# Kernel tuning notes

Measured on AMD Instinct MI355X. Metric: run time of the kernel, lower is better.

The kernel has to match this reference:

```python
import jax, jax.numpy as jnp
import numpy as np

B, N, HID = 2, 512, 768
BIAF = 256
CLS = 14
CH = 32
SIZE_DIM = 25
N_POS = 30
HSZ = 2 * (BIAF + 1) + SIZE_DIM


def setup_inputs() -> dict:
    key = jax.random.key(0)
    ks = jax.random.split(key, 16)
    s = 0.02
    return {
        "x": jax.random.normal(ks[0], (B, N, HID), jnp.float32),
        "y": jax.random.normal(ks[1], (B, N, HID), jnp.float32),
        "z": jax.random.normal(ks[2], (B, N, N, CH), jnp.float32),
        "mlp1_w": jax.random.normal(ks[3], (BIAF, HID), jnp.float32) * s,
        "mlp1_b": jnp.zeros((BIAF,), jnp.float32),
        "mlp2_w": jax.random.normal(ks[4], (BIAF, HID), jnp.float32) * s,
        "mlp2_b": jnp.zeros((BIAF,), jnp.float32),
        "head_w": jax.random.normal(ks[5], (BIAF, HID), jnp.float32) * s,
        "head_b": jnp.zeros((BIAF,), jnp.float32),
        "tail_w": jax.random.normal(ks[6], (BIAF, HID), jnp.float32) * s,
        "tail_b": jnp.zeros((BIAF,), jnp.float32),
        "biaf_W": jax.random.normal(ks[7], (CLS, BIAF + 1, BIAF + 1), jnp.float32) * s,
        "W": jax.random.normal(ks[8], (CLS, HSZ), jnp.float32) * s,
        "size_emb": jax.random.normal(ks[9], (N_POS, SIZE_DIM), jnp.float32) * s,
    }


def reference(x, y, z, mlp1_w, mlp1_b, mlp2_w, mlp2_b, head_w, head_b,
              tail_w, tail_b, biaf_W, W, size_emb):
    # MLP branches (dropout=0 at eval; torch GELU is exact erf)
    h = jax.nn.gelu(x @ mlp1_w.T + mlp1_b, approximate=False)   # (b,m,BIAF)
    t = jax.nn.gelu(y @ mlp2_w.T + mlp2_b, approximate=False)   # (b,n,BIAF)
    ones = jnp.ones(h.shape[:-1] + (1,), h.dtype)
    h1 = jnp.concatenate([h, ones], -1)                          # (b,m,BIAF+1)
    t1 = jnp.concatenate([t, ones], -1)                          # (b,n,BIAF+1)
    # Biaffine with bias_x=bias_y=True -> (b,cls,m,n)
    o1 = jnp.einsum('bmi,kij,bnj->bkmn', h1, biaf_W, t1)

    # head/tail MLPs with LeakyReLU(0.01), then append 1-column
    head = jax.nn.leaky_relu(x @ head_w.T + head_b, 0.01)
    tail = jax.nn.leaky_relu(x @ tail_w.T + tail_b, 0.01)
    head = jnp.concatenate([head, ones], -1)                     # (b,m,BIAF+1)
    tail = jnp.concatenate([tail, ones], -1)                     # (b,n,BIAF+1)

    # einsum('bmnh,kh->bkmn', cat([head_m, tail_n, size_mn]), W) decomposed so
    # the (b,m,n,HSZ) pairwise tensor is never materialized (same math).
    d = head.shape[-1]
    Wh, Wt, Ws = W[:, :d], W[:, d:2 * d], W[:, 2 * d:]
    n = x.shape[1]
    ar = jnp.arange(n)
    ids = jnp.clip(ar[None, :] - ar[:, None], -N_POS // 2, N_POS // 2 - 1) + N_POS // 2
    se = size_emb[ids]                                           # (m,n,SIZE_DIM)
    o3 = (jnp.einsum('bmh,kh->bkm', head, Wh)[:, :, :, None]
          + jnp.einsum('bnh,kh->bkn', tail, Wt)[:, :, None, :]
          + jnp.einsum('mnh,kh->kmn', se, Ws)[None])
    return o1 + o3
```

## Files before the change

### kernel.cpp

```cpp
#include <hip/hip_runtime.h>
#include <hip/hip_bf16.h>
#include <math.h>

#define BDIM 2
#define NDIM 512
#define HID 768
#define BIAF 256
#define CLS 14
#define DD 257
#define NPOS 30
#define SDIM 25
#define HSZ 539
#define PK 288
#define PJ 384

typedef unsigned short ushort_t;
typedef __attribute__((ext_vector_type(8))) short short8;
typedef __attribute__((ext_vector_type(4))) float floatx4;

#define MFMA16(a, b, c) __builtin_amdgcn_mfma_f32_16x16x32_bf16((a), (b), (c), 0, 0, 0)

__device__ inline float bf2f(ushort_t u) {
    union { unsigned int i; float f; } c; c.i = ((unsigned)u) << 16; return c.f;
}
__device__ inline ushort_t f2bf(float f) {
    __hip_bfloat16 h = __float2bfloat16(f);
    return *(ushort_t*)&h;
}

__device__ inline void split8(const float* v, short8& hi, short8& lo) {
    #pragma unroll
    for (int j = 0; j < 8; ++j) {
        ushort_t h = f2bf(v[j]);
        float hf = bf2f(h);
        ((short*)&hi)[j] = (short)h;
        ((short*)&lo)[j] = (short)f2bf(v[j] - hf);
    }
}

__global__ __launch_bounds__(256) void repack_t(
    const float* __restrict__ biafW, ushort_t* __restrict__ packW)
{
    __shared__ float tile[32][33];
    const int i0 = blockIdx.x * 32;
    const int j0 = blockIdx.y * 32;
    const int k  = blockIdx.z;
    const int r8 = threadIdx.x >> 5;
    const int c  = threadIdx.x & 31;
    #pragma unroll
    for (int rr = 0; rr < 4; ++rr) {
        int r = rr * 8 + r8;
        int gi = i0 + r, gj = j0 + c;
        tile[r][c] = (gi < DD && gj < DD) ? biafW[((size_t)k * DD + gi) * DD + gj] : 0.f;
    }
    __syncthreads();
    #pragma unroll
    for (int rr = 0; rr < 4; ++rr) {
        int jr = rr * 8 + r8;
        packW[((size_t)k * PJ + (j0 + jr)) * PK + i0 + c] = f2bf(tile[c][jr]);
    }
}

__global__ void fill_pads(ushort_t* __restrict__ h1hi, ushort_t* __restrict__ h1lo,
                          ushort_t* __restrict__ t1hi, ushort_t* __restrict__ t1lo) {
    int idx = blockIdx.x * 256 + threadIdx.x;
    int plane = idx >> 15;
    int tok = (idx >> 5) & 1023;
    int c   = 256 + (idx & 31);
    ushort_t* dst = (plane == 0) ? h1hi : (plane == 1) ? h1lo : (plane == 2) ? t1hi : t1lo;
    ushort_t val = (c == 256 && (plane == 0 || plane == 2)) ? (ushort_t)0x3F80 : (ushort_t)0;
    dst[(size_t)tok * PK + c] = val;
}

__global__ __launch_bounds__(256) void proj_mfma(
    const float* __restrict__ x, const float* __restrict__ y,
    const float* __restrict__ m1w, const float* __restrict__ m1b,
    const float* __restrict__ m2w, const float* __restrict__ m2b,
    const float* __restrict__ hw,  const float* __restrict__ hb,
    const float* __restrict__ tw,  const float* __restrict__ tb,
    ushort_t* __restrict__ h1hi, ushort_t* __restrict__ h1lo,
    ushort_t* __restrict__ t1hi, ushort_t* __restrict__ t1lo,
    float* __restrict__ headf, float* __restrict__ tailf)
{
    const int bx = blockIdx.x;
    const int proj = bx >> 6;
    const int mt = (bx >> 2) & 15;
    const int ft = bx & 3;
    const int wave = threadIdx.x >> 6, L = threadIdx.x & 63;
    const int quad = L >> 4, l16 = L & 15;
    const int m0w = mt * 64 + wave * 16;
    const int f0 = ft * 64;

    const float* src  = (proj == 1) ? y : x;
    const float* wmat = (proj == 0) ? m1w : (proj == 1) ? m2w : (proj == 2) ? hw : tw;
    const float* bias = (proj == 0) ? m1b : (proj == 1) ? m2b : (proj == 2) ? hb : tb;

    const float* arow = src + (size_t)(m0w + l16) * HID + quad * 8;

    floatx4 acc[4];
    #pragma unroll
    for (int nf = 0; nf < 4; ++nf)
        #pragma unroll
        for (int r = 0; r < 4; ++r) acc[nf][r] = 0.f;

    for (int k0 = 0; k0 < HID; k0 += 32) {
        float av[8];
        *(float4*)&av[0] = *(const float4*)(arow + k0);
        *(float4*)&av[4] = *(const float4*)(arow + k0 + 4);
        short8 ahi, alo;
        split8(av, ahi, alo);
        #pragma unroll
        for (int nf = 0; nf < 4; ++nf) {
            const float* brow = wmat + (size_t)(f0 + nf * 16 + l16) * HID + quad * 8 + k0;
            float bv[8];
            *(float4*)&bv[0] = *(const float4*)(brow);
            *(float4*)&bv[4] = *(const float4*)(brow + 4);
            short8 bhi, blo;
            split8(bv, bhi, blo);
            acc[nf] = MFMA16(ahi, bhi, acc[nf]);
            acc[nf] = MFMA16(alo, bhi, acc[nf]);
            acc[nf] = MFMA16(ahi, blo, acc[nf]);
        }
    }

    #pragma unroll
    for (int nf = 0; nf < 4; ++nf) {
        int feat = f0 + nf * 16 + l16;
        float bv = bias[feat];
        #pragma unroll
        for (int r = 0; r < 4; ++r) {
            int tok = m0w + quad * 4 + r;
            float v = acc[nf][r] + bv;
            if (proj == 0) {
                float g = 0.5f * v * (1.0f + erff(v * 0.70710678118654752f));
                ushort_t h = f2bf(g);
                h1hi[(size_t)tok * PK + feat] = h;
                h1lo[(size_t)tok * PK + feat] = f2bf(g - bf2f(h));
            } else if (proj == 1) {
                float g = 0.5f * v * (1.0f + erff(v * 0.70710678118654752f));
                ushort_t h = f2bf(g);
                t1hi[(size_t)tok * PK + feat] = h;
                t1lo[(size_t)tok * PK + feat] = f2bf(g - bf2f(h));
            } else if (proj == 2) {
                headf[(size_t)tok * 256 + feat] = (v >= 0.f) ? v : 0.01f * v;
            } else {
                tailf[(size_t)tok * 256 + feat] = (v >= 0.f) ? v : 0.01f * v;
            }
        }
    }
}

__global__ __launch_bounds__(256) void hk_tk_kernel(
    const float* __restrict__ headf, const float* __restrict__ tailf,
    const float* __restrict__ W,
    float* __restrict__ hk, float* __restrict__ tk)
{
    int p = blockIdx.x * 256 + threadIdx.x;
    int which = p >> 14;
    int idx = p & 16383;
    int tok = idx >> 4;
    int k = idx & 15;
    if (k >= CLS) return;
    const float* row = (which ? tailf : headf) + (size_t)tok * 256;
    const float* wr = W + (size_t)k * HSZ + (which ? DD : 0);
    float acc = 0.f;
    for (int f4 = 0; f4 < 64; ++f4) {
        float4 rv = *(const float4*)(row + f4 * 4);
        acc += rv.x * wr[f4*4] + rv.y * wr[f4*4+1] + rv.z * wr[f4*4+2] + rv.w * wr[f4*4+3];
    }
    acc += wr[256];
    float* dst = which ? tk : hk;
    dst[(size_t)(tok >> 9) * CLS * NDIM + (size_t)k * NDIM + (tok & 511)] = acc;
}

__global__ void sk_kernel(const float* __restrict__ semb, const float* __restrict__ W,
                          float* __restrict__ sk)
{
    int idx = blockIdx.x * 256 + threadIdx.x;
    if (idx < CLS * NPOS) {
        int k = idx / NPOS, d = idx % NPOS;
        float acc = 0.f;
        for (int h = 0; h < SDIM; ++h)
            acc += semb[d*SDIM + h] * W[k*HSZ + 2*DD + h];
        sk[idx] = acc;
    }
}

__global__ __launch_bounds__(256) void mb_mfma(
    const ushort_t* __restrict__ h1hi, const ushort_t* __restrict__ h1lo,
    const ushort_t* __restrict__ packW,
    ushort_t* __restrict__ Ab)
{
    const int jt = blockIdx.x, mt = blockIdx.y, bk = blockIdx.z;
    const int b = bk / CLS, k = bk % CLS;
    const int wave = threadIdx.x >> 6, L = threadIdx.x & 63;
    const int quad = L >> 4, l16 = L & 15;
    const int m0 = mt * 128 + (wave >> 1) * 64;
    const int j0 = jt * 128 + (wave & 1) * 64;
    const size_t abase = (size_t)b * NDIM * PK;
    const ushort_t* BT = packW + (size_t)k * PJ * PK;

    size_t aoff[4]; size_t boff[4];
    #pragma unroll
    for (int i = 0; i < 4; ++i) aoff[i] = abase + (size_t)(m0 + i * 16 + l16) * PK + quad * 8;
    #pragma unroll
    for (int i = 0; i < 4; ++i) boff[i] = (size_t)(j0 + i * 16 + l16) * PK + quad * 8;

    floatx4 acc[4][4];
    #pragma unroll
    for (int mi = 0; mi < 4; ++mi)
        #pragma unroll
        for (int ni = 0; ni < 4; ++ni)
            #pragma unroll
            for (int r = 0; r < 4; ++r) acc[mi][ni][r] = 0.f;

    for (int k0 = 0; k0 < PK; k0 += 32) {
        short8 ahi[4], alo[4], bb[4];
        #pragma unroll
        for (int i = 0; i < 4; ++i) {
            ahi[i] = *(const short8*)(h1hi + aoff[i] + k0);
            alo[i] = *(const short8*)(h1lo + aoff[i] + k0);
            bb[i]  = *(const short8*)(BT + boff[i] + k0);
        }
        #pragma unroll
        for (int mi = 0; mi < 4; ++mi)
            #pragma unroll
            for (int ni = 0; ni < 4; ++ni) {
                acc[mi][ni] = MFMA16(ahi[mi], bb[ni], acc[mi][ni]);
                acc[mi][ni] = MFMA16(alo[mi], bb[ni], acc[mi][ni]);
            }
    }

    ushort_t* Aout = Ab + (size_t)bk * NDIM * PK;
    #pragma unroll
    for (int mi = 0; mi < 4; ++mi) {
        #pragma unroll
        for (int r = 0; r < 4; ++r) {
            int row = m0 + mi * 16 + quad * 4 + r;
            #pragma unroll
            for (int ni = 0; ni < 4; ++ni) {
                int col = j0 + ni * 16 + l16;
                if (col < PK) Aout[(size_t)row * PK + col] = f2bf(acc[mi][ni][r]);
            }
        }
    }
}

__global__ __launch_bounds__(256) void mo_mfma(
    const ushort_t* __restrict__ Ab,
    const ushort_t* __restrict__ t1hi, const ushort_t* __restrict__ t1lo,
    const float* __restrict__ hk, const float* __restrict__ tk,
    const float* __restrict__ sk,
    float* __restrict__ out)
{
    __shared__ float skr[NPOS];
    const int nt = blockIdx.x, mt = blockIdx.y, bk = blockIdx.z;
    const int b = bk / CLS, k = bk % CLS;
    if (threadIdx.x < NPOS) skr[threadIdx.x] = sk[k * NPOS + threadIdx.x];
    __syncthreads();
    const int wave = threadIdx.x >> 6, L = threadIdx.x & 63;
    const int quad = L >> 4, l16 = L & 15;
    const int m0 = mt * 128 + (wave >> 1) * 64;
    const int n0 = nt * 128 + (wave & 1) * 64;
    const ushort_t* A = Ab + (size_t)bk * NDIM * PK;
    const size_t tbase = (size_t)b * NDIM * PK;

    size_t aoff[4]; size_t boff[4];
    #pragma unroll
    for (int i = 0; i < 4; ++i) aoff[i] = (size_t)(m0 + i * 16 + l16) * PK + quad * 8;
    #pragma unroll
    for (int i = 0; i < 4; ++i) boff[i] = tbase + (size_t)(n0 + i * 16 + l16) * PK + quad * 8;

    floatx4 acc[4][4];
    #pragma unroll
    for (int mi = 0; mi < 4; ++mi)
        #pragma unroll
        for (int ni = 0; ni < 4; ++ni)
            #pragma unroll
            for (int r = 0; r < 4; ++r) acc[mi][ni][r] = 0.f;

    for (int k0 = 0; k0 < PK; k0 += 32) {
        short8 a[4], bhi[4], blo[4];
        #pragma unroll
        for (int i = 0; i < 4; ++i) {
            a[i]   = *(const short8*)(A + aoff[i] + k0);
            bhi[i] = *(const short8*)(t1hi + boff[i] + k0);
            blo[i] = *(const short8*)(t1lo + boff[i] + k0);
        }
        #pragma unroll
        for (int mi = 0; mi < 4; ++mi)
            #pragma unroll
            for (int ni = 0; ni < 4; ++ni) {
                acc[mi][ni] = MFMA16(a[mi], bhi[ni], acc[mi][ni]);
                acc[mi][ni] = MFMA16(a[mi], blo[ni], acc[mi][ni]);
            }
    }

    const size_t obase = (size_t)bk * NDIM;
    #pragma unroll
    for (int mi = 0; mi < 4; ++mi) {
        #pragma unroll
        for (int r = 0; r < 4; ++r) {
            int row = m0 + mi * 16 + quad * 4 + r;
            float hv = hk[obase + row];
            #pragma unroll
            for (int ni = 0; ni < 4; ++ni) {
                int col = n0 + ni * 16 + l16;
                int d = col - row; d = d < -15 ? -15 : (d > 14 ? 14 : d); d += 15;
                out[(obase + row) * NDIM + col] = acc[mi][ni][r] + hv + tk[obase + col] + skr[d];
            }
        }
    }
}

extern "C" void kernel_launch(void* const* d_in, const int* in_sizes, int n_in,
                              void* d_out, int out_size, void* d_ws, size_t ws_size,
                              hipStream_t stream) {
    const float* x    = (const float*)d_in[0];
    const float* y    = (const float*)d_in[1];
    const float* m1w  = (const float*)d_in[3];
    const float* m1b  = (const float*)d_in[4];
    const float* m2w  = (const float*)d_in[5];
    const float* m2b  = (const float*)d_in[6];
    const float* hw   = (const float*)d_in[7];
    const float* hb   = (const float*)d_in[8];
    const float* tw   = (const float*)d_in[9];
    const float* tb   = (const float*)d_in[10];
    const float* biafW= (const float*)d_in[11];
    const float* W    = (const float*)d_in[12];
    const float* semb = (const float*)d_in[13];

    char* p = (char*)d_ws;
    float* hk   = (float*)p;                    p += 57344;
    float* tk   = (float*)p;                    p += 57344;
    float* skp  = (float*)p;                    p += 2048;
    float* headf= (float*)p;                    p += 1048576;
    float* tailf= (float*)p;                    p += 1048576;
    ushort_t* h1hi = (ushort_t*)p;              p += 589824;
    ushort_t* h1lo = (ushort_t*)p;              p += 589824;
    ushort_t* t1hi = (ushort_t*)p;              p += 589824;
    ushort_t* t1lo = (ushort_t*)p;              p += 589824;
    ushort_t* packW= (ushort_t*)p;              p += 3096576;
    ushort_t* Abuf = (ushort_t*)p;              p += 8257536;

    repack_t<<<dim3(9, 12, CLS), 256, 0, stream>>>(biafW, packW);
    fill_pads<<<512, 256, 0, stream>>>(h1hi, h1lo, t1hi, t1lo);
    proj_mfma<<<256, 256, 0, stream>>>(x, y, m1w, m1b, m2w, m2b,
                                       hw, hb, tw, tb,
                                       h1hi, h1lo, t1hi, t1lo, headf, tailf);
    hk_tk_kernel<<<128, 256, 0, stream>>>(headf, tailf, W, hk, tk);
    sk_kernel<<<2, 256, 0, stream>>>(semb, W, skp);
    mb_mfma<<<dim3(3, 4, BDIM*CLS), 256, 0, stream>>>(h1hi, h1lo, packW, Abuf);
    mo_mfma<<<dim3(4, 4, BDIM*CLS), 256, 0, stream>>>(Abuf, t1hi, t1lo, hk, tk, skp,
                                                      (float*)d_out);
}
```

Baseline: 217.1 us.

## Fuse biaffine stages via LDS intermediate and pre-split projection weights to bf16

Merges the two biaffine GEMM kernels into one kernel. Each block computes a 64-row slice of h1·W_k into shared memory, then multiplies it by t1 directly, so the global bf16 intermediate buffer and one launch are gone. It also adds a kernel that pre-splits the four projection weight matrices into bf16 hi/lo planes, so proj_mfma loads them instead of converting per block. In exchange, the first stage is now recomputed for every 64-row slice at full width, giving a smaller grid (224 blocks) with more registers per wave. The per-wave column assignment is also uneven (5 vs 4 fragments).

Result: slower. 259.5 us (+19.5%).

```diff
diff --git a/kernel.cpp b/kernel.cpp
--- a/kernel.cpp
+++ b/kernel.cpp
@@ -61,6 +61,21 @@
     }
 }
 
+__global__ __launch_bounds__(256) void wsplit(
+    const float* __restrict__ m1w, const float* __restrict__ m2w,
+    const float* __restrict__ hw,  const float* __restrict__ tw,
+    ushort_t* __restrict__ whi, ushort_t* __restrict__ wlo)
+{
+    int idx = blockIdx.x * 256 + threadIdx.x;
+    int mat = idx / (BIAF * HID);
+    int rem = idx % (BIAF * HID);
+    const float* src = (mat == 0) ? m1w : (mat == 1) ? m2w : (mat == 2) ? hw : tw;
+    float v = src[rem];
+    ushort_t h = f2bf(v);
+    whi[idx] = h;
+    wlo[idx] = f2bf(v - bf2f(h));
+}
+
 __global__ void fill_pads(ushort_t* __restrict__ h1hi, ushort_t* __restrict__ h1lo,
                           ushort_t* __restrict__ t1hi, ushort_t* __restrict__ t1lo) {
     int idx = blockIdx.x * 256 + threadIdx.x;
@@ -74,10 +89,9 @@
 
 __global__ __launch_bounds__(256) void proj_mfma(
     const float* __restrict__ x, const float* __restrict__ y,
-    const float* __restrict__ m1w, const float* __restrict__ m1b,
-    const float* __restrict__ m2w, const float* __restrict__ m2b,
-    const float* __restrict__ hw,  const float* __restrict__ hb,
-    const float* __restrict__ tw,  const float* __restrict__ tb,
+    const ushort_t* __restrict__ whi, const ushort_t* __restrict__ wlo,
+    const float* __restrict__ m1b, const float* __restrict__ m2b,
+    const float* __restrict__ hb,  const float* __restrict__ tb,
     ushort_t* __restrict__ h1hi, ushort_t* __restrict__ h1lo,
     ushort_t* __restrict__ t1hi, ushort_t* __restrict__ t1lo,
     float* __restrict__ headf, float* __restrict__ tailf)
@@ -92,10 +106,10 @@
     const int f0 = ft * 64;
 
     const float* src  = (proj == 1) ? y : x;
-    const float* wmat = (proj == 0) ? m1w : (proj == 1) ? m2w : (proj == 2) ? hw : tw;
     const float* bias = (proj == 0) ? m1b : (proj == 1) ? m2b : (proj == 2) ? hb : tb;
 
     const float* arow = src + (size_t)(m0w + l16) * HID + quad * 8;
+    const size_t wbase = (size_t)proj * BIAF * HID;
 
     floatx4 acc[4];
     #pragma unroll
@@ -111,12 +125,9 @@
         split8(av, ahi, alo);
         #pragma unroll
         for (int nf = 0; nf < 4; ++nf) {
-            const float* brow = wmat + (size_t)(f0 + nf * 16 + l16) * HID + quad * 8 + k0;
-            float bv[8];
-            *(float4*)&bv[0] = *(const float4*)(brow);
-            *(float4*)&bv[4] = *(const float4*)(brow + 4);
-            short8 bhi, blo;
-            split8(bv, bhi, blo);
+            size_t boff = wbase + (size_t)(f0 + nf * 16 + l16) * HID + quad * 8 + k0;
+            short8 bhi = *(const short8*)(whi + boff);
+            short8 blo = *(const short8*)(wlo + boff);
             acc[nf] = MFMA16(ahi, bhi, acc[nf]);
             acc[nf] = MFMA16(alo, bhi, acc[nf]);
             acc[nf] = MFMA16(ahi, blo, acc[nf]);
@@ -186,114 +197,109 @@
     }
 }
 
-__global__ __launch_bounds__(256) void mb_mfma(
+__global__ __launch_bounds__(256) void fused_out(
     const ushort_t* __restrict__ h1hi, const ushort_t* __restrict__ h1lo,
     const ushort_t* __restrict__ packW,
-    ushort_t* __restrict__ Ab)
-{
-    const int jt = blockIdx.x, mt = blockIdx.y, bk = blockIdx.z;
-    const int b = bk / CLS, k = bk % CLS;
-    const int wave = threadIdx.x >> 6, L = threadIdx.x & 63;
-    const int quad = L >> 4, l16 = L & 15;
-    const int m0 = mt * 128 + (wave >> 1) * 64;
-    const int j0 = jt * 128 + (wave & 1) * 64;
-    const size_t abase = (size_t)b * NDIM * PK;
-    const ushort_t* BT = packW + (size_t)k * PJ * PK;
-
-    size_t aoff[4]; size_t boff[4];
-    #pragma unroll
-    for (int i = 0; i < 4; ++i) aoff[i] = abase + (size_t)(m0 + i * 16 + l16) * PK + quad * 8;
-    #pragma unroll
-    for (int i = 0; i < 4; ++i) boff[i] = (size_t)(j0 + i * 16 + l16) * PK + quad * 8;
-
-    floatx4 acc[4][4];
-    #pragma unroll
-    for (int mi = 0; mi < 4; ++mi)
-        #pragma unroll
-        for (int ni = 0; ni < 4; ++ni)
-            #pragma unroll
-            for (int r = 0; r < 4; ++r) acc[mi][ni][r] = 0.f;
-
-    for (int k0 = 0; k0 < PK; k0 += 32) {
-        short8 ahi[4], alo[4], bb[4];
-        #pragma unroll
-        for (int i = 0; i < 4; ++i) {
-            ahi[i] = *(const short8*)(h1hi + aoff[i] + k0);
-            alo[i] = *(const short8*)(h1lo + aoff[i] + k0);
-            bb[i]  = *(const short8*)(BT + boff[i] + k0);
-        }
-        #pragma unroll
-        for (int mi = 0; mi < 4; ++mi)
-            #pragma unroll
-            for (int ni = 0; ni < 4; ++ni) {
-                acc[mi][ni] = MFMA16(ahi[mi], bb[ni], acc[mi][ni]);
-                acc[mi][ni] = MFMA16(alo[mi], bb[ni], acc[mi][ni]);
-            }
-    }
-
-    ushort_t* Aout = Ab + (size_t)bk * NDIM * PK;
-    #pragma unroll
-    for (int mi = 0; mi < 4; ++mi) {
-        #pragma unroll
-        for (int r = 0; r < 4; ++r) {
-            int row = m0 + mi * 16 + quad * 4 + r;
-            #pragma unroll
-            for (int ni = 0; ni < 4; ++ni) {
-                int col = j0 + ni * 16 + l16;
-                if (col < PK) Aout[(size_t)row * PK + col] = f2bf(acc[mi][ni][r]);
-            }
-        }
-    }
-}
-
-__global__ __launch_bounds__(256) void mo_mfma(
-    const ushort_t* __restrict__ Ab,
     const ushort_t* __restrict__ t1hi, const ushort_t* __restrict__ t1lo,
     const float* __restrict__ hk, const float* __restrict__ tk,
     const float* __restrict__ sk,
     float* __restrict__ out)
 {
+    __shared__ ushort_t Alds[64][PK];
     __shared__ float skr[NPOS];
-    const int nt = blockIdx.x, mt = blockIdx.y, bk = blockIdx.z;
+    const int mt = blockIdx.x, bk = blockIdx.y;
     const int b = bk / CLS, k = bk % CLS;
-    if (threadIdx.x < NPOS) skr[threadIdx.x] = sk[k * NPOS + threadIdx.x];
-    __syncthreads();
     const int wave = threadIdx.x >> 6, L = threadIdx.x & 63;
     const int quad = L >> 4, l16 = L & 15;
-    const int m0 = mt * 128 + (wave >> 1) * 64;
-    const int n0 = nt * 128 + (wave & 1) * 64;
-    const ushort_t* A = Ab + (size_t)bk * NDIM * PK;
+    const int m0 = mt * 64;
+    if (threadIdx.x < NPOS) skr[threadIdx.x] = sk[k * NPOS + threadIdx.x];
+
+    {
+        const size_t h1base = (size_t)b * NDIM * PK;
+        const ushort_t* BT = packW + (size_t)k * PJ * PK;
+        size_t aoff[4];
+        #pragma unroll
+        for (int mi = 0; mi < 4; ++mi)
+            aoff[mi] = h1base + (size_t)(m0 + mi * 16 + l16) * PK + quad * 8;
+
+        int jfs[5]; int njf = 0;
+        for (int jf = wave; jf < 18; jf += 4) jfs[njf++] = jf;
+
+        floatx4 acc1[4][5];
+        #pragma unroll
+        for (int mi = 0; mi < 4; ++mi)
+            #pragma unroll
+            for (int jj = 0; jj < 5; ++jj)
+                #pragma unroll
+                for (int r = 0; r < 4; ++r) acc1[mi][jj][r] = 0.f;
+
+        for (int k0 = 0; k0 < PK; k0 += 32) {
+            short8 ahi[4], alo[4];
+            #pragma unroll
+            for (int mi = 0; mi < 4; ++mi) {
+                ahi[mi] = *(const short8*)(h1hi + aoff[mi] + k0);
+                alo[mi] = *(const short8*)(h1lo + aoff[mi] + k0);
+            }
+            for (int jj = 0; jj < njf; ++jj) {
+                short8 bb = *(const short8*)(BT + (size_t)(jfs[jj] * 16 + l16) * PK + quad * 8 + k0);
+                #pragma unroll
+                for (int mi = 0; mi < 4; ++mi) {
+                    acc1[mi][jj] = MFMA16(ahi[mi], bb, acc1[mi][jj]);
+                    acc1[mi][jj] = MFMA16(alo[mi], bb, acc1[mi][jj]);
+                }
+            }
+        }
+        for (int jj = 0; jj < njf; ++jj) {
+            int j0 = jfs[jj] * 16;
+            #pragma unroll
+            for (int mi = 0; mi < 4; ++mi)
+                #pragma unroll
+                for (int r = 0; r < 4; ++r)
+                    Alds[mi * 16 + quad * 4 + r][j0 + l16] = f2bf(acc1[mi][jj][r]);
+        }
+    }
+    __syncthreads();
+
+    const int n0 = wave * 128;
     const size_t tbase = (size_t)b * NDIM * PK;
-
-    size_t aoff[4]; size_t boff[4];
-    #pragma unroll
-    for (int i = 0; i < 4; ++i) aoff[i] = (size_t)(m0 + i * 16 + l16) * PK + quad * 8;
-    #pragma unroll
-    for (int i = 0; i < 4; ++i) boff[i] = tbase + (size_t)(n0 + i * 16 + l16) * PK + quad * 8;
-
-    floatx4 acc[4][4];
+    size_t boff[8];
+    #pragma unroll
+    for (int nf = 0; nf < 8; ++nf)
+        boff[nf] = tbase + (size_t)(n0 + nf * 16 + l16) * PK + quad * 8;
+
+    floatx4 acc2[4][8];
     #pragma unroll
     for (int mi = 0; mi < 4; ++mi)
         #pragma unroll
-        for (int ni = 0; ni < 4; ++ni)
-            #pragma unroll
-            for (int r = 0; r < 4; ++r) acc[mi][ni][r] = 0.f;
+        for (int nf = 0; nf < 8; ++nf)
+            #pragma unroll
+            for (int r = 0; r < 4; ++r) acc2[mi][nf][r] = 0.f;
 
     for (int k0 = 0; k0 < PK; k0 += 32) {
-        short8 a[4], bhi[4], blo[4];
-        #pragma unroll
-        for (int i = 0; i < 4; ++i) {
-            a[i]   = *(const short8*)(A + aoff[i] + k0);
-            bhi[i] = *(const short8*)(t1hi + boff[i] + k0);
-            blo[i] = *(const short8*)(t1lo + boff[i] + k0);
-        }
+        short8 a[4];
         #pragma unroll
         for (int mi = 0; mi < 4; ++mi)
-            #pragma unroll
-            for (int ni = 0; ni < 4; ++ni) {
-                acc[mi][ni] = MFMA16(a[mi], bhi[ni], acc[mi][ni]);
-                acc[mi][ni] = MFMA16(a[mi], blo[ni], acc[mi][ni]);
-            }
+            a[mi] = *(const short8*)&Alds[mi * 16 + l16][k0 + quad * 8];
+        {
+            short8 bh[8];
+            #pragma unroll
+            for (int nf = 0; nf < 8; ++nf) bh[nf] = *(const short8*)(t1hi + boff[nf] + k0);
+            #pragma unroll
+            for (int mi = 0; mi < 4; ++mi)
+                #pragma unroll
+                for (int nf = 0; nf < 8; ++nf)
+                    acc2[mi][nf] = MFMA16(a[mi], bh[nf], acc2[mi][nf]);
+        }
+        {
+            short8 bl[8];
+            #pragma unroll
+            for (int nf = 0; nf < 8; ++nf) bl[nf] = *(const short8*)(t1lo + boff[nf] + k0);
+            #pragma unroll
+            for (int mi = 0; mi < 4; ++mi)
+                #pragma unroll
+                for (int nf = 0; nf < 8; ++nf)
+                    acc2[mi][nf] = MFMA16(a[mi], bl[nf], acc2[mi][nf]);
+        }
     }
 
     const size_t obase = (size_t)bk * NDIM;
@@ -304,10 +310,10 @@
             int row = m0 + mi * 16 + quad * 4 + r;
             float hv = hk[obase + row];
             #pragma unroll
-            for (int ni = 0; ni < 4; ++ni) {
-                int col = n0 + ni * 16 + l16;
+            for (int nf = 0; nf < 8; ++nf) {
+                int col = n0 + nf * 16 + l16;
                 int d = col - row; d = d < -15 ? -15 : (d > 14 ? 14 : d); d += 15;
-                out[(obase + row) * NDIM + col] = acc[mi][ni][r] + hv + tk[obase + col] + skr[d];
+                out[(obase + row) * NDIM + col] = acc2[mi][nf][r] + hv + tk[obase + col] + skr[d];
             }
         }
     }
@@ -341,16 +347,16 @@
     ushort_t* t1hi = (ushort_t*)p;              p += 589824;
     ushort_t* t1lo = (ushort_t*)p;              p += 589824;
     ushort_t* packW= (ushort_t*)p;              p += 3096576;
-    ushort_t* Abuf = (ushort_t*)p;              p += 8257536;
+    ushort_t* whi  = (ushort_t*)p;              p += 1572864;
+    ushort_t* wlo  = (ushort_t*)p;              p += 1572864;
 
     repack_t<<<dim3(9, 12, CLS), 256, 0, stream>>>(biafW, packW);
+    wsplit<<<3072, 256, 0, stream>>>(m1w, m2w, hw, tw, whi, wlo);
     fill_pads<<<512, 256, 0, stream>>>(h1hi, h1lo, t1hi, t1lo);
-    proj_mfma<<<256, 256, 0, stream>>>(x, y, m1w, m1b, m2w, m2b,
-                                       hw, hb, tw, tb,
+    proj_mfma<<<256, 256, 0, stream>>>(x, y, whi, wlo, m1b, m2b, hb, tb,
                                        h1hi, h1lo, t1hi, t1lo, headf, tailf);
     hk_tk_kernel<<<128, 256, 0, stream>>>(headf, tailf, W, hk, tk);
     sk_kernel<<<2, 256, 0, stream>>>(semb, W, skp);
-    mb_mfma<<<dim3(3, 4, BDIM*CLS), 256, 0, stream>>>(h1hi, h1lo, packW, Abuf);
-    mo_mfma<<<dim3(4, 4, BDIM*CLS), 256, 0, stream>>>(Abuf, t1hi, t1lo, hk, tk, skp,
-                                                      (float*)d_out);
-}
+    fused_out<<<dim3(8, BDIM*CLS), 256, 0, stream>>>(h1hi, h1lo, packW, t1hi, t1lo,
+                                                     hk, tk, skp, (float*)d_out);
+}
```

## Stage GEMM tiles through LDS and pre-split projection weights to bf16

Applied to the files above, without the earlier changes.

The two biaffine GEMM kernels now copy each 128x32 A and B tile into padded shared memory once per block. The four waves then read their fragments from there instead of each loading overlapping rows straight from global memory. Separately, a new wsplit kernel converts the four projection weight matrices to bf16 hi/lo halves once, so proj_mfma loads ready-made bf16 fragments instead of re-splitting fp32 weights in every block. This adds an extra kernel launch, two barriers per k-step, and about 3 MB of workspace, and there is no double buffering, so loads and MFMAs do not overlap.

After: 214.5 us. Within noise of the previous version (-1.2%).

```diff
diff --git a/kernel.cpp b/kernel.cpp
--- a/kernel.cpp
+++ b/kernel.cpp
@@ -13,6 +13,7 @@
 #define HSZ 539
 #define PK 288
 #define PJ 384
+#define LDW 40
 
 typedef unsigned short ushort_t;
 typedef __attribute__((ext_vector_type(8))) short short8;
@@ -35,6 +36,17 @@
         float hf = bf2f(h);
         ((short*)&hi)[j] = (short)h;
         ((short*)&lo)[j] = (short)f2bf(v[j] - hf);
+    }
+}
+
+__device__ inline void stage_tile(const ushort_t* __restrict__ g, size_t gstride,
+                                  ushort_t* __restrict__ lds, int tid) {
+    int r0 = tid >> 2, c4 = tid & 3;
+    #pragma unroll
+    for (int i = 0; i < 2; ++i) {
+        int row = i * 64 + r0;
+        uint4 v = *(const uint4*)(g + (size_t)row * gstride + c4 * 8);
+        *(uint4*)(lds + row * LDW + c4 * 8) = v;
     }
 }
 
@@ -59,6 +71,21 @@
         int jr = rr * 8 + r8;
         packW[((size_t)k * PJ + (j0 + jr)) * PK + i0 + c] = f2bf(tile[c][jr]);
     }
+}
+
+__global__ __launch_bounds__(256) void wsplit(
+    const float* __restrict__ m1w, const float* __restrict__ m2w,
+    const float* __restrict__ hw,  const float* __restrict__ tw,
+    ushort_t* __restrict__ whi, ushort_t* __restrict__ wlo)
+{
+    int idx = blockIdx.x * 256 + threadIdx.x;
+    int mat = idx / (BIAF * HID);
+    int rem = idx % (BIAF * HID);
+    const float* src = (mat == 0) ? m1w : (mat == 1) ? m2w : (mat == 2) ? hw : tw;
+    float v = src[rem];
+    ushort_t h = f2bf(v);
+    whi[idx] = h;
+    wlo[idx] = f2bf(v - bf2f(h));
 }
 
 __global__ void fill_pads(ushort_t* __restrict__ h1hi, ushort_t* __restrict__ h1lo,
@@ -74,10 +101,9 @@
 
 __global__ __launch_bounds__(256) void proj_mfma(
     const float* __restrict__ x, const float* __restrict__ y,
-    const float* __restrict__ m1w, const float* __restrict__ m1b,
-    const float* __restrict__ m2w, const float* __restrict__ m2b,
-    const float* __restrict__ hw,  const float* __restrict__ hb,
-    const float* __restrict__ tw,  const float* __restrict__ tb,
+    const ushort_t* __restrict__ whi, const ushort_t* __restrict__ wlo,
+    const float* __restrict__ m1b, const float* __restrict__ m2b,
+    const float* __restrict__ hb,  const float* __restrict__ tb,
     ushort_t* __restrict__ h1hi, ushort_t* __restrict__ h1lo,
     ushort_t* __restrict__ t1hi, ushort_t* __restrict__ t1lo,
     float* __restrict__ headf, float* __restrict__ tailf)
@@ -92,10 +118,10 @@
     const int f0 = ft * 64;
 
     const float* src  = (proj == 1) ? y : x;
-    const float* wmat = (proj == 0) ? m1w : (proj == 1) ? m2w : (proj == 2) ? hw : tw;
     const float* bias = (proj == 0) ? m1b : (proj == 1) ? m2b : (proj == 2) ? hb : tb;
 
     const float* arow = src + (size_t)(m0w + l16) * HID + quad * 8;
+    const size_t wbase = (size_t)proj * BIAF * HID;
 
     floatx4 acc[4];
     #pragma unroll
@@ -111,12 +137,9 @@
         split8(av, ahi, alo);
         #pragma unroll
         for (int nf = 0; nf < 4; ++nf) {
-            const float* brow = wmat + (size_t)(f0 + nf * 16 + l16) * HID + quad * 8 + k0;
-            float bv[8];
-            *(float4*)&bv[0] = *(const float4*)(brow);
-            *(float4*)&bv[4] = *(const float4*)(brow + 4);
-            short8 bhi, blo;
-            split8(bv, bhi, blo);
+            size_t boff = wbase + (size_t)(f0 + nf * 16 + l16) * HID + quad * 8 + k0;
+            short8 bhi = *(const short8*)(whi + boff);
+            short8 blo = *(const short8*)(wlo + boff);
             acc[nf] = MFMA16(ahi, bhi, acc[nf]);
             acc[nf] = MFMA16(alo, bhi, acc[nf]);
             acc[nf] = MFMA16(ahi, blo, acc[nf]);
@@ -186,25 +209,29 @@
     }
 }
 
-__global__ __launch_bounds__(256) void mb_mfma(
+__global__ __launch_bounds__(256) void mb_tile(
     const ushort_t* __restrict__ h1hi, const ushort_t* __restrict__ h1lo,
     const ushort_t* __restrict__ packW,
     ushort_t* __restrict__ Ab)
 {
+    __shared__ ushort_t lds[3 * 128 * LDW];
+    ushort_t* Ahi = lds;
+    ushort_t* Alo = lds + 128 * LDW;
+    ushort_t* Bt  = lds + 2 * 128 * LDW;
+
     const int jt = blockIdx.x, mt = blockIdx.y, bk = blockIdx.z;
     const int b = bk / CLS, k = bk % CLS;
-    const int wave = threadIdx.x >> 6, L = threadIdx.x & 63;
+    const int tid = threadIdx.x;
+    const int wave = tid >> 6, L = tid & 63;
     const int quad = L >> 4, l16 = L & 15;
-    const int m0 = mt * 128 + (wave >> 1) * 64;
-    const int j0 = jt * 128 + (wave & 1) * 64;
-    const size_t abase = (size_t)b * NDIM * PK;
-    const ushort_t* BT = packW + (size_t)k * PJ * PK;
-
-    size_t aoff[4]; size_t boff[4];
-    #pragma unroll
-    for (int i = 0; i < 4; ++i) aoff[i] = abase + (size_t)(m0 + i * 16 + l16) * PK + quad * 8;
-    #pragma unroll
-    for (int i = 0; i < 4; ++i) boff[i] = (size_t)(j0 + i * 16 + l16) * PK + quad * 8;
+    const int m0 = mt * 128;
+    const int j0 = jt * 128;
+    const int wm = (wave >> 1) * 64;
+    const int wn = (wave & 1) * 64;
+
+    const ushort_t* gA_hi = h1hi + (size_t)(b * NDIM + m0) * PK;
+    const ushort_t* gA_lo = h1lo + (size_t)(b * NDIM + m0) * PK;
+    const ushort_t* gB    = packW + ((size_t)k * PJ + j0) * PK;
 
     floatx4 acc[4][4];
     #pragma unroll
@@ -215,12 +242,16 @@
             for (int r = 0; r < 4; ++r) acc[mi][ni][r] = 0.f;
 
     for (int k0 = 0; k0 < PK; k0 += 32) {
+        stage_tile(gA_hi + k0, PK, Ahi, tid);
+        stage_tile(gA_lo + k0, PK, Alo, tid);
+        stage_tile(gB + k0, PK, Bt, tid);
+        __syncthreads();
         short8 ahi[4], alo[4], bb[4];
         #pragma unroll
         for (int i = 0; i < 4; ++i) {
-            ahi[i] = *(const short8*)(h1hi + aoff[i] + k0);
-            alo[i] = *(const short8*)(h1lo + aoff[i] + k0);
-            bb[i]  = *(const short8*)(BT + boff[i] + k0);
+            ahi[i] = *(const short8*)(Ahi + (wm + i * 16 + l16) * LDW + quad * 8);
+            alo[i] = *(const short8*)(Alo + (wm + i * 16 + l16) * LDW + quad * 8);
+            bb[i]  = *(const short8*)(Bt  + (wn + i * 16 + l16) * LDW + quad * 8);
         }
         #pragma unroll
         for (int mi = 0; mi < 4; ++mi)
@@ -229,6 +260,7 @@
                 acc[mi][ni] = MFMA16(ahi[mi], bb[ni], acc[mi][ni]);
                 acc[mi][ni] = MFMA16(alo[mi], bb[ni], acc[mi][ni]);
             }
+        __syncthreads();
     }
 
     ushort_t* Aout = Ab + (size_t)bk * NDIM * PK;
@@ -236,40 +268,43 @@
     for (int mi = 0; mi < 4; ++mi) {
         #pragma unroll
         for (int r = 0; r < 4; ++r) {
-            int row = m0 + mi * 16 + quad * 4 + r;
+            int row = m0 + wm + mi * 16 + quad * 4 + r;
             #pragma unroll
             for (int ni = 0; ni < 4; ++ni) {
-                int col = j0 + ni * 16 + l16;
+                int col = j0 + wn + ni * 16 + l16;
                 if (col < PK) Aout[(size_t)row * PK + col] = f2bf(acc[mi][ni][r]);
             }
         }
     }
 }
 
-__global__ __launch_bounds__(256) void mo_mfma(
+__global__ __launch_bounds__(256) void mo_tile(
     const ushort_t* __restrict__ Ab,
     const ushort_t* __restrict__ t1hi, const ushort_t* __restrict__ t1lo,
     const float* __restrict__ hk, const float* __restrict__ tk,
     const float* __restrict__ sk,
     float* __restrict__ out)
 {
+    __shared__ ushort_t lds[3 * 128 * LDW];
     __shared__ float skr[NPOS];
+    ushort_t* At  = lds;
+    ushort_t* Bhi = lds + 128 * LDW;
+    ushort_t* Blo = lds + 2 * 128 * LDW;
+
     const int nt = blockIdx.x, mt = blockIdx.y, bk = blockIdx.z;
     const int b = bk / CLS, k = bk % CLS;
-    if (threadIdx.x < NPOS) skr[threadIdx.x] = sk[k * NPOS + threadIdx.x];
-    __syncthreads();
-    const int wave = threadIdx.x >> 6, L = threadIdx.x & 63;
+    const int tid = threadIdx.x;
+    if (tid < NPOS) skr[tid] = sk[k * NPOS + tid];
+    const int wave = tid >> 6, L = tid & 63;
     const int quad = L >> 4, l16 = L & 15;
-    const int m0 = mt * 128 + (wave >> 1) * 64;
-    const int n0 = nt * 128 + (wave & 1) * 64;
-    const ushort_t* A = Ab + (size_t)bk * NDIM * PK;
-    const size_t tbase = (size_t)b * NDIM * PK;
-
-    size_t aoff[4]; size_t boff[4];
-    #pragma unroll
-    for (int i = 0; i < 4; ++i) aoff[i] = (size_t)(m0 + i * 16 + l16) * PK + quad * 8;
-    #pragma unroll
-    for (int i = 0; i < 4; ++i) boff[i] = tbase + (size_t)(n0 + i * 16 + l16) * PK + quad * 8;
+    const int m0 = mt * 128;
+    const int n0 = nt * 128;
+    const int wm = (wave >> 1) * 64;
+    const int wn = (wave & 1) * 64;
+
+    const ushort_t* gA  = Ab + ((size_t)bk * NDIM + m0) * PK;
+    const ushort_t* gBh = t1hi + (size_t)(b * NDIM + n0) * PK;
+    const ushort_t* gBl = t1lo + (size_t)(b * NDIM + n0) * PK;
 
     floatx4 acc[4][4];
     #pragma unroll
@@ -280,20 +315,25 @@
             for (int r = 0; r < 4; ++r) acc[mi][ni][r] = 0.f;
 
     for (int k0 = 0; k0 < PK; k0 += 32) {
-        short8 a[4], bhi[4], blo[4];
+        stage_tile(gA + k0, PK, At, tid);
+        stage_tile(gBh + k0, PK, Bhi, tid);
+        stage_tile(gBl + k0, PK, Blo, tid);
+        __syncthreads();
+        short8 a[4], bh[4], bl[4];
         #pragma unroll
         for (int i = 0; i < 4; ++i) {
-            a[i]   = *(const short8*)(A + aoff[i] + k0);
-            bhi[i] = *(const short8*)(t1hi + boff[i] + k0);
-            blo[i] = *(const short8*)(t1lo + boff[i] + k0);
+            a[i]  = *(const short8*)(At  + (wm + i * 16 + l16) * LDW + quad * 8);
+            bh[i] = *(const short8*)(Bhi + (wn + i * 16 + l16) * LDW + quad * 8);
+            bl[i] = *(const short8*)(Blo + (wn + i * 16 + l16) * LDW + quad * 8);
         }
         #pragma unroll
         for (int mi = 0; mi < 4; ++mi)
             #pragma unroll
             for (int ni = 0; ni < 4; ++ni) {
-                acc[mi][ni] = MFMA16(a[mi], bhi[ni], acc[mi][ni]);
-                acc[mi][ni] = MFMA16(a[mi], blo[ni], acc[mi][ni]);
-            }
+                acc[mi][ni] = MFMA16(a[mi], bh[ni], acc[mi][ni]);
+                acc[mi][ni] = MFMA16(a[mi], bl[ni], acc[mi][ni]);
+            }
+        __syncthreads();
     }
 
     const size_t obase = (size_t)bk * NDIM;
@@ -301,11 +341,11 @@
     for (int mi = 0; mi < 4; ++mi) {
         #pragma unroll
         for (int r = 0; r < 4; ++r) {
-            int row = m0 + mi * 16 + quad * 4 + r;
+            int row = m0 + wm + mi * 16 + quad * 4 + r;
             float hv = hk[obase + row];
             #pragma unroll
             for (int ni = 0; ni < 4; ++ni) {
-                int col = n0 + ni * 16 + l16;
+                int col = n0 + wn + ni * 16 + l16;
                 int d = col - row; d = d < -15 ? -15 : (d > 14 ? 14 : d); d += 15;
                 out[(obase + row) * NDIM + col] = acc[mi][ni][r] + hv + tk[obase + col] + skr[d];
             }
@@ -341,16 +381,18 @@
     ushort_t* t1hi = (ushort_t*)p;              p += 589824;
     ushort_t* t1lo = (ushort_t*)p;              p += 589824;
     ushort_t* packW= (ushort_t*)p;              p += 3096576;
+    ushort_t* whi  = (ushort_t*)p;              p += 1572864;
+    ushort_t* wlo  = (ushort_t*)p;              p += 1572864;
     ushort_t* Abuf = (ushort_t*)p;              p += 8257536;
 
     repack_t<<<dim3(9, 12, CLS), 256, 0, stream>>>(biafW, packW);
+    wsplit<<<3072, 256, 0, stream>>>(m1w, m2w, hw, tw, whi, wlo);
     fill_pads<<<512, 256, 0, stream>>>(h1hi, h1lo, t1hi, t1lo);
-    proj_mfma<<<256, 256, 0, stream>>>(x, y, m1w, m1b, m2w, m2b,
-                                       hw, hb, tw, tb,
+    proj_mfma<<<256, 256, 0, stream>>>(x, y, whi, wlo, m1b, m2b, hb, tb,
                                        h1hi, h1lo, t1hi, t1lo, headf, tailf);
     hk_tk_kernel<<<128, 256, 0, stream>>>(headf, tailf, W, hk, tk);
     sk_kernel<<<2, 256, 0, stream>>>(semb, W, skp);
-    mb_mfma<<<dim3(3, 4, BDIM*CLS), 256, 0, stream>>>(h1hi, h1lo, packW, Abuf);
-    mo_mfma<<<dim3(4, 4, BDIM*CLS), 256, 0, stream>>>(Abuf, t1hi, t1lo, hk, tk, skp,
+    mb_tile<<<dim3(3, 4, BDIM*CLS), 256, 0, stream>>>(h1hi, h1lo, packW, Abuf);
+    mo_tile<<<dim3(4, 4, BDIM*CLS), 256, 0, stream>>>(Abuf, t1hi, t1lo, hk, tk, skp,
                                                       (float*)d_out);
 }
```
